# Kernel optimization log

Measured on AMD Instinct MI355X. Metric: run time of the kernel, lower is better.

## Reference

```python
import jax, jax.numpy as jnp
import numpy as np

N = 256            # state_space_size
BF = (4, 4, 4)     # branching_factors
T = 128            # time steps
D_IN = 64          # input_size
D_T = 64           # time_embedding_size
BATCH = 16
NUM_NODES = N * 4 * 4 * 4  # 16384


def setup_inputs() -> dict:
    key = jax.random.key(0)
    ks = jax.random.split(key, 20)

    def lin_w(k, out_d, in_d):
        return jax.random.normal(k, (out_d, in_d), jnp.float32) / np.sqrt(in_d)

    inp = {
        "x": jax.random.normal(ks[0], (BATCH, T, N), jnp.float32),
        "t_embeddings_schedule": jax.random.normal(ks[1], (T, D_T), jnp.float32),
        "input_vector": jax.random.normal(ks[2], (BATCH, T, D_IN), jnp.float32),
        # Fanout node params
        "Wa": lin_w(ks[3], NUM_NODES, N),
        "ba": jnp.zeros((NUM_NODES,), jnp.float32),
        "Wt": lin_w(ks[4], NUM_NODES, D_T),
        "Wi": lin_w(ks[5], NUM_NODES, D_IN),
        # Node with bf[:3]=[4,4,4]: reduces last 4 -> [N,4,4]
        "w3": jax.random.normal(ks[6], (N, 4, 4, 4), jnp.float32) * np.sqrt(2.0 / (4 + N * 16)),
        "tW3": lin_w(ks[7], N * 16, D_T),
        "tb3": jnp.zeros((N * 16,), jnp.float32),
        # Node with bf[:2]=[4,4]
        "w2": jax.random.normal(ks[8], (N, 4, 4), jnp.float32) * np.sqrt(2.0 / (4 + N * 4)),
        "tW2": lin_w(ks[9], N * 4, D_T),
        "tb2": jnp.zeros((N * 4,), jnp.float32),
        # Node with bf[:1]=[4]
        "w1": jax.random.normal(ks[10], (N, 4), jnp.float32) * np.sqrt(2.0 / (4 + N)),
        "tW1": lin_w(ks[11], N, D_T),
        "tb1": jnp.zeros((N,), jnp.float32),
    }
    return inp


def _node(act, t_emb, w, tW, tb):
    # act: [..., T, N, *bf]; w: [N, *bf]; reduce last branching dim
    tproj = (t_emb @ tW.T + tb).reshape(t_emb.shape[0], *w.shape[:-1])  # [T, N, *bf[:-1]]
    pre = (w * act).sum(-1) + tproj  # broadcast over leading batch dims
    return jax.nn.softplus(pre)


def reference(x, t_embeddings_schedule, input_vector, Wa, ba, Wt, Wi,
              w3, tW3, tb3, w2, tW2, tb2, w1, tW1, tb1):
    t_emb = t_embeddings_schedule
    # Fanout: [B, T, N] -> [B, T, N, 4, 4, 4]
    pre = x @ Wa.T + ba + (t_emb @ Wt.T) + input_vector @ Wi.T  # [B, T, NUM_NODES]
    act = jax.nn.softplus(pre.reshape(*pre.shape[:-1], N, *BF))
    # Tree: deepest node first (insert-at-1 order in original)
    act = _node(act, t_emb, w3, tW3, tb3)  # [B, T, N, 4, 4]
    act = _node(act, t_emb, w2, tW2, tb2)  # [B, T, N, 4]
    act = _node(act, t_emb, w1, tW1, tb1)  # [B, T, N]
    return act
```

## Files before the change

### kernel.cpp

```cpp
#include <hip/hip_runtime.h>

typedef __attribute__((ext_vector_type(16))) float f32x16;
typedef __attribute__((ext_vector_type(8))) __bf16 bf16x8;
typedef __attribute__((ext_vector_type(8))) unsigned short u16x8;

__device__ __forceinline__ unsigned short f2bf(float f) {
    unsigned int u = __float_as_uint(f);
    u += 0x7fffu + ((u >> 16) & 1u);
    return (unsigned short)(u >> 16);
}

__device__ __forceinline__ float softplus_f(float x) {
    float e = __expf(-fabsf(x));
    return fmaxf(x, 0.0f) + __logf(1.0f + e);
}

typedef __attribute__((address_space(3))) void lds_void_t;
typedef __attribute__((address_space(1))) void glb_void_t;

__device__ __forceinline__ void load16_to_lds(const void* g, const void* l) {
    __builtin_amdgcn_global_load_lds((glb_void_t*)(unsigned long long)g,
                                     (lds_void_t*)(unsigned int)(unsigned long long)l,
                                     16, 0, 0);
}

#define REPACK_NB 2
#define REPACK_BLOCKS 1728
__global__ __launch_bounds__(256) void repack(
        const float* __restrict__ x, const float* __restrict__ iv,
        const float* __restrict__ temb,
        const float* __restrict__ Wa, const float* __restrict__ Wi,
        const float* __restrict__ Wt,
        unsigned short* __restrict__ Abf ) {
    const int stride = REPACK_BLOCKS * 256;
    const int tid0 = blockIdx.x * 256 + threadIdx.x;
    float4 f[REPACK_NB][2];
    #pragma unroll
    for (int c = 0; c < REPACK_NB; ++c) {
        const int idx = tid0 + c * stride;
        const bool isA = idx < 98304;
        const int widx = isA ? idx : idx - 98304;
        const int row = widx / 48;
        const int kk  = (widx % 48) * 8;
        const float* p0 = isA ? (x    + (size_t)row * 256) : (Wa + (size_t)row * 256);
        const float* p1 = isA ? (iv   + (size_t)row * 64)  : (Wi + (size_t)row * 64);
        const float* p2 = isA ? (temb + (size_t)(row & 127) * 64) : (Wt + (size_t)row * 64);
        const float* src = (kk < 256) ? (p0 + kk) : ((kk < 320) ? (p1 + kk - 256) : (p2 + kk - 320));
        f[c][0] = ((const float4*)src)[0];
        f[c][1] = ((const float4*)src)[1];
    }
    #pragma unroll
    for (int c = 0; c < REPACK_NB; ++c) {
        const int idx = tid0 + c * stride;
        u16x8 o;
        o[0] = f2bf(f[c][0].x); o[1] = f2bf(f[c][0].y); o[2] = f2bf(f[c][0].z); o[3] = f2bf(f[c][0].w);
        o[4] = f2bf(f[c][1].x); o[5] = f2bf(f[c][1].y); o[6] = f2bf(f[c][1].z); o[7] = f2bf(f[c][1].w);
        *(u16x8*)(Abf + (size_t)idx * 8) = o;
    }
}

__global__ __launch_bounds__(256) void tproj(
        const float* __restrict__ temb,
        const float* __restrict__ tW3, const float* __restrict__ tb3,
        const float* __restrict__ tW2, const float* __restrict__ tb2,
        const float* __restrict__ tW1, const float* __restrict__ tb1,
        float* __restrict__ tp3T, float* __restrict__ tp2T, float* __restrict__ tp1T) {
    __shared__ float se[32 * 64];
    const int tid = threadIdx.x;
    const int tbase = blockIdx.y * 32;
    for (int i = tid; i < 32 * 64; i += 256) se[i] = temb[tbase * 64 + i];
    __syncthreads();
    const int j = blockIdx.x * 64 + (tid >> 2);
    const float* W; const float* bias; float* outp; int jl;
    if      (j < 4096) { W = tW3; bias = tb3; outp = tp3T; jl = j; }
    else if (j < 5120) { W = tW2; bias = tb2; outp = tp2T; jl = j - 4096; }
    else               { W = tW1; bias = tb1; outp = tp1T; jl = j - 5120; }
    float4 wreg[16];
    const float4* wrow = (const float4*)(W + (size_t)jl * 64);
    #pragma unroll
    for (int k = 0; k < 16; ++k) wreg[k] = wrow[k];
    const float b = bias[jl];
    #pragma unroll
    for (int s = 0; s < 8; ++s) {
        const int tl = (tid & 3) + s * 4;
        const float4* e4 = (const float4*)&se[tl * 64];
        float a = b;
        #pragma unroll
        for (int k = 0; k < 16; ++k) {
            float4 e = e4[k];
            a += wreg[k].x * e.x + wreg[k].y * e.y + wreg[k].z * e.z + wreg[k].w * e.w;
        }
        outp[(size_t)jl * 128 + tbase + tl] = a;
    }
}

__global__ __launch_bounds__(256, 3)
void fused_gemm_tree(const unsigned short* __restrict__ Wbf,
                     const unsigned short* __restrict__ Abf,
                     const float* __restrict__ ba,
                     const float* __restrict__ tp3T, const float* __restrict__ tp2T,
                     const float* __restrict__ tp1T,
                     const float* __restrict__ w3, const float* __restrict__ w2,
                     const float* __restrict__ w1,
                     float* __restrict__ out) {
    __shared__ unsigned short sW[128 * 64];
    __shared__ unsigned short sA[128 * 64];

    const int tid  = threadIdx.x;
    const int wave = tid >> 6;
    const int lane = tid & 63;
    const int wr = wave >> 1;
    const int wc = wave & 1;
    const int lane31 = lane & 31;
    const int h = lane >> 5;

    const int node0 = blockIdx.x * 128;
    const int m0    = blockIdx.y * 128;

    f32x16 acc[2][2];
    #pragma unroll
    for (int fm = 0; fm < 2; ++fm)
        #pragma unroll
        for (int cf = 0; cf < 2; ++cf)
            #pragma unroll
            for (int r = 0; r < 16; ++r) acc[fm][cf][r] = 0.0f;

    const unsigned short* aBase = Wbf + (size_t)node0 * 384;
    const unsigned short* bBase = Abf + (size_t)m0 * 384;

    const int wrow0 = wr * 64 + lane31;
    const int arow0 = wc * 64 + lane31;

    for (int k0 = 0; k0 < 384; k0 += 64) {
        __syncthreads();
        #pragma unroll
        for (int rr = 0; rr < 4; ++rr) {
            const int p = rr * 256 + tid;
            const int row = p >> 3;
            const int kchunk = (p & 7) ^ (row & 7);
            const size_t soff = (size_t)row * 384 + k0 + kchunk * 8;
            load16_to_lds(aBase + soff, &sW[(size_t)(rr * 256 + wave * 64) * 8]);
            load16_to_lds(bBase + soff, &sA[(size_t)(rr * 256 + wave * 64) * 8]);
        }
        __syncthreads();

        #pragma unroll
        for (int s = 0; s < 4; ++s) {
            const int kc = s * 2 + h;
            bf16x8 af[2], bf[2];
            #pragma unroll
            for (int fm = 0; fm < 2; ++fm) {
                const int row = wrow0 + fm * 32;
                af[fm] = *(const bf16x8*)&sW[row * 64 + (kc ^ (row & 7)) * 8];
            }
            #pragma unroll
            for (int cf = 0; cf < 2; ++cf) {
                const int row = arow0 + cf * 32;
                bf[cf] = *(const bf16x8*)&sA[row * 64 + (kc ^ (row & 7)) * 8];
            }
            #pragma unroll
            for (int fm = 0; fm < 2; ++fm)
                #pragma unroll
                for (int cf = 0; cf < 2; ++cf)
                    acc[fm][cf] = __builtin_amdgcn_mfma_f32_32x32x16_bf16(af[fm], bf[cf], acc[fm][cf], 0, 0, 0);
        }
    }

    const int n = blockIdx.x * 2 + wr;
    const int t0 = wc * 64 + lane31;

    float4 bav[2][4], w3v[2][4];
    #pragma unroll
    for (int fm = 0; fm < 2; ++fm)
        #pragma unroll
        for (int s2 = 0; s2 < 4; ++s2) {
            const int leafbase = fm * 32 + 8 * s2 + 4 * h;
            bav[fm][s2] = *(const float4*)&ba[node0 + wr * 64 + leafbase];
            w3v[fm][s2] = *(const float4*)&w3[n * 64 + leafbase];
        }
    float w2v[4][2], w1v[4];
    #pragma unroll
    for (int i = 0; i < 4; ++i) {
        #pragma unroll
        for (int s2b = 0; s2b < 2; ++s2b)
            w2v[i][s2b] = w2[n * 16 + i * 4 + 2 * s2b + h];
        w1v[i] = w1[n * 4 + i];
    }
    float tp3v[2][2][4], tp2v[2][2][2], tp1v[2];
    #pragma unroll
    for (int fm = 0; fm < 2; ++fm)
        #pragma unroll
        for (int cf = 0; cf < 2; ++cf) {
            const int t = t0 + cf * 32;
            #pragma unroll
            for (int s2 = 0; s2 < 4; ++s2) {
                const int i  = fm * 2 + (s2 >> 1);
                const int jj = 2 * (s2 & 1) + h;
                tp3v[fm][cf][s2] = tp3T[(size_t)((n * 4 + i) * 4 + jj) * 128 + t];
            }
            #pragma unroll
            for (int b = 0; b < 2; ++b)
                tp2v[fm][cf][b] = tp2T[(size_t)(n * 4 + fm * 2 + b) * 128 + t];
        }
    #pragma unroll
    for (int cf = 0; cf < 2; ++cf) tp1v[cf] = tp1T[(size_t)n * 128 + t0 + cf * 32];

    float s1[2] = {0.0f, 0.0f};
    #pragma unroll
    for (int fm = 0; fm < 2; ++fm) {
        #pragma unroll
        for (int cf = 0; cf < 2; ++cf) {
            #pragma unroll
            for (int b = 0; b < 2; ++b) {
                float cs = 0.0f;
                #pragma unroll
                for (int s2b = 0; s2b < 2; ++s2b) {
                    const int s2 = 2 * b + s2b;
                    float p3 = 0.0f;
                    const float* bv = (const float*)&bav[fm][s2];
                    const float* wv = (const float*)&w3v[fm][s2];
                    #pragma unroll
                    for (int l = 0; l < 4; ++l) {
                        float a0 = softplus_f(acc[fm][cf][s2 * 4 + l] + bv[l]);
                        p3 = fmaf(a0, wv[l], p3);
                    }
                    float a3 = softplus_f(p3 + tp3v[fm][cf][s2]);
                    cs = fmaf(a3, w2v[fm * 2 + b][s2b], cs);
                }
                float Q = cs + __shfl_xor(cs, 32);
                float a2 = softplus_f(Q + tp2v[fm][cf][b]);
                s1[cf] = fmaf(a2, w1v[fm * 2 + b], s1[cf]);
            }
        }
    }
    {
        const float sj = h ? s1[1] : s1[0];
        const float tq = h ? tp1v[1] : tp1v[0];
        const int t = t0 + h * 32;
        out[(size_t)(m0 + t) * 256 + n] = softplus_f(sj + tq);
    }
}

extern "C" void kernel_launch(void* const* d_in, const int* in_sizes, int n_in,
                              void* d_out, int out_size, void* d_ws, size_t ws_size,
                              hipStream_t stream) {
    const float* x    = (const float*)d_in[0];
    const float* temb = (const float*)d_in[1];
    const float* iv   = (const float*)d_in[2];
    const float* Wa   = (const float*)d_in[3];
    const float* ba   = (const float*)d_in[4];
    const float* Wt   = (const float*)d_in[5];
    const float* Wi   = (const float*)d_in[6];
    const float* w3   = (const float*)d_in[7];
    const float* tW3  = (const float*)d_in[8];
    const float* tb3  = (const float*)d_in[9];
    const float* w2   = (const float*)d_in[10];
    const float* tW2  = (const float*)d_in[11];
    const float* tb2  = (const float*)d_in[12];
    const float* w1   = (const float*)d_in[13];
    const float* tW1  = (const float*)d_in[14];
    const float* tb1  = (const float*)d_in[15];
    float* out = (float*)d_out;

    char* ws = (char*)d_ws;
    unsigned short* Abf = (unsigned short*)(ws);
    unsigned short* Wbf = (unsigned short*)(ws + 1572864);
    float* tp3T = (float*)(ws + 14155776);
    float* tp2T = (float*)(ws + 16252928);
    float* tp1T = (float*)(ws + 16777216);

    repack<<<dim3(REPACK_BLOCKS), dim3(256), 0, stream>>>(x, iv, temb, Wa, Wi, Wt, Abf);
    tproj<<<dim3(84, 4), dim3(256), 0, stream>>>(temb, tW3, tb3, tW2, tb2, tW1, tb1,
                                                 tp3T, tp2T, tp1T);
    fused_gemm_tree<<<dim3(128, 16), dim3(256), 0, stream>>>(Wbf, Abf, ba, tp3T, tp2T, tp1T,
                                                             w3, w2, w1, out);
}
```

Measured before the change: 155.8 us.

## Pre-tile operands into MFMA fragment order and load directly to registers

The repack kernel now writes the bf16 activation and weight matrices in a layout where each wave's 32x16 MFMA fragment is a contiguous 1 KB chunk. The GEMM loop drops the LDS staging and barriers and has each wave load its fragments straight from global memory into registers. This removes the LDS round trips and __syncthreads per K step. In exchange, fragments that two waves share are each fetched twice from global/L2, and global-load latency must be hidden without double buffering.

Result: slower. 160.8 us (+3.2%).

```diff
diff --git a/kernel.cpp b/kernel.cpp
--- a/kernel.cpp
+++ b/kernel.cpp
@@ -13,15 +13,6 @@
 __device__ __forceinline__ float softplus_f(float x) {
     float e = __expf(-fabsf(x));
     return fmaxf(x, 0.0f) + __logf(1.0f + e);
-}
-
-typedef __attribute__((address_space(3))) void lds_void_t;
-typedef __attribute__((address_space(1))) void glb_void_t;
-
-__device__ __forceinline__ void load16_to_lds(const void* g, const void* l) {
-    __builtin_amdgcn_global_load_lds((glb_void_t*)(unsigned long long)g,
-                                     (lds_void_t*)(unsigned int)(unsigned long long)l,
-                                     16, 0, 0);
 }
 
 #define REPACK_NB 2
@@ -31,31 +22,38 @@
         const float* __restrict__ temb,
         const float* __restrict__ Wa, const float* __restrict__ Wi,
         const float* __restrict__ Wt,
-        unsigned short* __restrict__ Abf ) {
+        unsigned short* __restrict__ Abf2 ) {
     const int stride = REPACK_BLOCKS * 256;
     const int tid0 = blockIdx.x * 256 + threadIdx.x;
     float4 f[REPACK_NB][2];
+    int dsto[REPACK_NB];
     #pragma unroll
     for (int c = 0; c < REPACK_NB; ++c) {
         const int idx = tid0 + c * stride;
         const bool isA = idx < 98304;
         const int widx = isA ? idx : idx - 98304;
         const int row = widx / 48;
-        const int kk  = (widx % 48) * 8;
+        const int kc  = widx % 48;
+        const int kk  = kc * 8;
         const float* p0 = isA ? (x    + (size_t)row * 256) : (Wa + (size_t)row * 256);
         const float* p1 = isA ? (iv   + (size_t)row * 64)  : (Wi + (size_t)row * 64);
         const float* p2 = isA ? (temb + (size_t)(row & 127) * 64) : (Wt + (size_t)row * 64);
         const float* src = (kk < 256) ? (p0 + kk) : ((kk < 320) ? (p1 + kk - 256) : (p2 + kk - 320));
         f[c][0] = ((const float4*)src)[0];
         f[c][1] = ((const float4*)src)[1];
+        const int g  = row >> 5;
+        const int r31 = row & 31;
+        const int kp = kc >> 1;
+        const int h  = kc & 1;
+        const int o  = ((g * 24 + kp) * 64) + h * 32 + r31;
+        dsto[c] = (isA ? o : (98304 + o));
     }
     #pragma unroll
     for (int c = 0; c < REPACK_NB; ++c) {
-        const int idx = tid0 + c * stride;
         u16x8 o;
         o[0] = f2bf(f[c][0].x); o[1] = f2bf(f[c][0].y); o[2] = f2bf(f[c][0].z); o[3] = f2bf(f[c][0].w);
         o[4] = f2bf(f[c][1].x); o[5] = f2bf(f[c][1].y); o[6] = f2bf(f[c][1].z); o[7] = f2bf(f[c][1].w);
-        *(u16x8*)(Abf + (size_t)idx * 8) = o;
+        *(u16x8*)(Abf2 + (size_t)dsto[c] * 8) = o;
     }
 }
 
@@ -95,17 +93,14 @@
 }
 
 __global__ __launch_bounds__(256, 3)
-void fused_gemm_tree(const unsigned short* __restrict__ Wbf,
-                     const unsigned short* __restrict__ Abf,
+void fused_gemm_tree(const unsigned short* __restrict__ Wbf2,
+                     const unsigned short* __restrict__ Abf2,
                      const float* __restrict__ ba,
                      const float* __restrict__ tp3T, const float* __restrict__ tp2T,
                      const float* __restrict__ tp1T,
                      const float* __restrict__ w3, const float* __restrict__ w2,
                      const float* __restrict__ w1,
                      float* __restrict__ out) {
-    __shared__ unsigned short sW[128 * 64];
-    __shared__ unsigned short sA[128 * 64];
-
     const int tid  = threadIdx.x;
     const int wave = tid >> 6;
     const int lane = tid & 63;
@@ -125,45 +120,23 @@
             #pragma unroll
             for (int r = 0; r < 16; ++r) acc[fm][cf][r] = 0.0f;
 
-    const unsigned short* aBase = Wbf + (size_t)node0 * 384;
-    const unsigned short* bBase = Abf + (size_t)m0 * 384;
-
-    const int wrow0 = wr * 64 + lane31;
-    const int arow0 = wc * 64 + lane31;
-
-    for (int k0 = 0; k0 < 384; k0 += 64) {
-        __syncthreads();
-        #pragma unroll
-        for (int rr = 0; rr < 4; ++rr) {
-            const int p = rr * 256 + tid;
-            const int row = p >> 3;
-            const int kchunk = (p & 7) ^ (row & 7);
-            const size_t soff = (size_t)row * 384 + k0 + kchunk * 8;
-            load16_to_lds(aBase + soff, &sW[(size_t)(rr * 256 + wave * 64) * 8]);
-            load16_to_lds(bBase + soff, &sA[(size_t)(rr * 256 + wave * 64) * 8]);
-        }
-        __syncthreads();
-
-        #pragma unroll
-        for (int s = 0; s < 4; ++s) {
-            const int kc = s * 2 + h;
-            bf16x8 af[2], bf[2];
-            #pragma unroll
-            for (int fm = 0; fm < 2; ++fm) {
-                const int row = wrow0 + fm * 32;
-                af[fm] = *(const bf16x8*)&sW[row * 64 + (kc ^ (row & 7)) * 8];
-            }
-            #pragma unroll
-            for (int cf = 0; cf < 2; ++cf) {
-                const int row = arow0 + cf * 32;
-                bf[cf] = *(const bf16x8*)&sA[row * 64 + (kc ^ (row & 7)) * 8];
-            }
-            #pragma unroll
-            for (int fm = 0; fm < 2; ++fm)
-                #pragma unroll
-                for (int cf = 0; cf < 2; ++cf)
-                    acc[fm][cf] = __builtin_amdgcn_mfma_f32_32x32x16_bf16(af[fm], bf[cf], acc[fm][cf], 0, 0, 0);
-        }
+    const unsigned short* aW0 = Wbf2 + (size_t)(blockIdx.x * 4 + wr * 2 + 0) * 24 * 512;
+    const unsigned short* aW1 = aW0 + 24 * 512;
+    const unsigned short* aA0 = Abf2 + (size_t)(blockIdx.y * 4 + wc * 2 + 0) * 24 * 512;
+    const unsigned short* aA1 = aA0 + 24 * 512;
+    const int lo = lane * 8;
+
+    #pragma unroll
+    for (int kp = 0; kp < 24; ++kp) {
+        const int off = kp * 512 + lo;
+        bf16x8 af0 = *(const bf16x8*)(aW0 + off);
+        bf16x8 af1 = *(const bf16x8*)(aW1 + off);
+        bf16x8 bf0 = *(const bf16x8*)(aA0 + off);
+        bf16x8 bf1 = *(const bf16x8*)(aA1 + off);
+        acc[0][0] = __builtin_amdgcn_mfma_f32_32x32x16_bf16(af0, bf0, acc[0][0], 0, 0, 0);
+        acc[0][1] = __builtin_amdgcn_mfma_f32_32x32x16_bf16(af0, bf1, acc[0][1], 0, 0, 0);
+        acc[1][0] = __builtin_amdgcn_mfma_f32_32x32x16_bf16(af1, bf0, acc[1][0], 0, 0, 0);
+        acc[1][1] = __builtin_amdgcn_mfma_f32_32x32x16_bf16(af1, bf1, acc[1][1], 0, 0, 0);
     }
 
     const int n = blockIdx.x * 2 + wr;
@@ -263,15 +236,15 @@
     float* out = (float*)d_out;
 
     char* ws = (char*)d_ws;
-    unsigned short* Abf = (unsigned short*)(ws);
-    unsigned short* Wbf = (unsigned short*)(ws + 1572864);
+    unsigned short* Abf2 = (unsigned short*)(ws);
+    unsigned short* Wbf2 = (unsigned short*)(ws + 1572864);
     float* tp3T = (float*)(ws + 14155776);
     float* tp2T = (float*)(ws + 16252928);
     float* tp1T = (float*)(ws + 16777216);
 
-    repack<<<dim3(REPACK_BLOCKS), dim3(256), 0, stream>>>(x, iv, temb, Wa, Wi, Wt, Abf);
+    repack<<<dim3(REPACK_BLOCKS), dim3(256), 0, stream>>>(x, iv, temb, Wa, Wi, Wt, Abf2);
     tproj<<<dim3(84, 4), dim3(256), 0, stream>>>(temb, tW3, tb3, tW2, tb2, tW1, tb1,
                                                  tp3T, tp2T, tp1T);
-    fused_gemm_tree<<<dim3(128, 16), dim3(256), 0, stream>>>(Wbf, Abf, ba, tp3T, tp2T, tp1T,
+    fused_gemm_tree<<<dim3(128, 16), dim3(256), 0, stream>>>(Wbf2, Abf2, ba, tp3T, tp2T, tp1T,
                                                              w3, w2, w1, out);
 }
```
